# Optimization experiments

Hardware: AMD Instinct MI355X
Metric: run time of the kernel (lower is better)

The kernel has to match this reference:

```python
import jax, jax.numpy as jnp
import numpy as np

PSP_SIZES = (1, 3, 6, 8)  # KV length S = 1 + 9 + 36 + 64 = 110
BN_EPS = 1e-5


def conv1x1(x, W, b):
    # x: [B,C,H,W], W: [O,C], b: [O] -> [B,O,H,W]
    return jnp.einsum('bchw,oc->bohw', x, W) + b[None, :, None, None]


def psp(f):
    # f: [B,C,H,W] -> [B,C,S]; H,W divisible by all sizes so adaptive pool == block mean
    B, C, H, W = f.shape
    priors = []
    for s in PSP_SIZES:
        p = f.reshape(B, C, s, H // s, s, W // s).mean(axis=(3, 5))  # [B,C,s,s]
        priors.append(p.reshape(B, C, s * s))
    return jnp.concatenate(priors, axis=-1)  # [B,C,S]


def setup_inputs() -> dict:
    key = jax.random.key(0)
    ks = jax.random.split(key, 8)
    B, C, H, W = 8, 512, 72, 72
    Kc, Vc = 256, 256
    return {
        'x': jax.random.normal(ks[0], (B, C, H, W), jnp.float32),
        'Wk': jax.random.normal(ks[1], (Kc, C), jnp.float32) * (1.0 / np.sqrt(C)),
        'bk': jax.random.normal(ks[2], (Kc,), jnp.float32) * 0.01,
        'gamma': jnp.ones((Kc,), jnp.float32),
        'beta': jnp.zeros((Kc,), jnp.float32),
        'rmean': jnp.zeros((Kc,), jnp.float32),
        'rvar': jax.random.uniform(ks[3], (Kc,), jnp.float32, 0.5, 1.5),
        'Wv': jax.random.normal(ks[4], (Vc, C), jnp.float32) * (1.0 / np.sqrt(C)),
        'bv': jax.random.normal(ks[5], (Vc,), jnp.float32) * 0.01,
        'Ww': jax.random.normal(ks[6], (C, Vc), jnp.float32) * (1.0 / np.sqrt(Vc)),
        'bw': jnp.zeros((C,), jnp.float32),
    }


def reference(x, Wk, bk, gamma, beta, rmean, rvar, Wv, bv, Ww, bw):
    B, C, H, W = x.shape
    Kc = Wk.shape[0]
    Vc = Wv.shape[0]
    # f_value: conv1x1, then PSP -> value [B,S,Vc]
    value = psp(conv1x1(x, Wv, bv)).transpose(0, 2, 1)
    # f_key == f_query: conv1x1 + BN(inference) + ReLU
    k = conv1x1(x, Wk, bk)
    inv = gamma / jnp.sqrt(rvar + BN_EPS)
    k = jax.nn.relu(k * inv[None, :, None, None] + (beta - rmean * inv)[None, :, None, None])
    query = k.reshape(B, Kc, H * W).transpose(0, 2, 1)  # [B,HW,Kc]
    keyt = psp(k)  # [B,Kc,S]
    sim = jnp.einsum('bnk,bks->bns', query, keyt) * (Kc ** -0.5)
    sim = jax.nn.softmax(sim, axis=-1)
    context = jnp.einsum('bns,bsv->bnv', sim, value)  # [B,HW,Vc]
    context = context.transpose(0, 2, 1).reshape(B, Vc, H, W)
    return conv1x1(context, Ww, bw)
```

## Files before the change

kernel.cpp:

```cpp
#include <hip/hip_runtime.h>
#include <hip/hip_bf16.h>

#define HW    5184
#define WIDTH 72
#define CIN   512
#define KC    256
#define VC    256
#define NS    110
#define NSP   112
#define SPV   128
#define BATCH 8

typedef unsigned short u16;
typedef unsigned int   u32;
typedef __attribute__((ext_vector_type(8))) short bf16x8;
typedef __attribute__((ext_vector_type(4))) float f32x4;

typedef const __attribute__((address_space(1))) u32* gp_t;
typedef __attribute__((address_space(3))) u32* lp_t;

__device__ __forceinline__ u32 f2bf1(float f) {
    u32 u = __float_as_uint(f);
    return (u + 0x7FFFu + ((u >> 16) & 1u)) >> 16;
}
__device__ __forceinline__ u32 pack2(float a, float b) {
    return f2bf1(a) | (f2bf1(b) << 16);
}

__global__ void prep_kernel(const float* __restrict__ bk, const float* __restrict__ gamma,
                            const float* __restrict__ beta, const float* __restrict__ rmean,
                            const float* __restrict__ rvar, float* __restrict__ inv_out,
                            float* __restrict__ bc_out) {
    int i = threadIdx.x;
    float inv = gamma[i] * rsqrtf(rvar[i] + 1e-5f);
    inv_out[i] = inv;
    bc_out[i]  = bk[i] * inv + beta[i] - rmean[i] * inv;
}

__global__ __launch_bounds__(256) void cvt_w_kernel(
    const float* __restrict__ Wk, const float* __restrict__ Ww, const float* __restrict__ Wv,
    u16* __restrict__ Wkbf, u16* __restrict__ Wwbf, u16* __restrict__ Wvbf)
{
    int j = (blockIdx.x * 256 + threadIdx.x) * 4;
    const float* s; u16* d;
    if (j < KC * CIN)          { s = Wk; d = Wkbf; }
    else if (j < 2 * KC * CIN) { j -= KC * CIN;     s = Ww; d = Wwbf; }
    else                       { j -= 2 * KC * CIN; s = Wv; d = Wvbf; }
    float4 v = *(const float4*)&s[j];
    uint2 u;
    u.x = pack2(v.x, v.y);
    u.y = pack2(v.z, v.w);
    *(uint2*)&d[j] = u;
}

__global__ __launch_bounds__(256) void transpose_cvt_kernel(
    const float* __restrict__ in, u16* __restrict__ out, int C)
{
    const int z  = blockIdx.z;
    const int n0 = blockIdx.x * 32;
    const int k0 = blockIdx.y * 32;
    __shared__ float t[32][33];
    const int tx = threadIdx.x & 31, ty = threadIdx.x >> 5;
    const float* src = in + ((size_t)z * C + k0) * HW + n0;
#pragma unroll
    for (int i = 0; i < 4; i++)
        t[ty + i * 8][tx] = src[(size_t)(ty + i * 8) * HW + tx];
    __syncthreads();
    u16* dst = out + ((size_t)z * HW + n0) * C + k0;
    const int kp  = (threadIdx.x & 15) * 2;
    const int nl0 = threadIdx.x >> 4;
#pragma unroll
    for (int j = 0; j < 2; j++) {
        int nl = nl0 + j * 16;
        u32 u = pack2(t[kp][nl], t[kp + 1][nl]);
        *(u32*)&dst[(size_t)nl * C + kp] = u;
    }
}

__global__ __launch_bounds__(256) void gemm_nt_bf16(
    const u16* __restrict__ A, const u16* __restrict__ B, float* __restrict__ C,
    u16* __restrict__ Ct,
    int M, int N, int K, int nbx, int nby,
    const float* __restrict__ scale, const float* __restrict__ bias, int relu)
{
    const int tot = nbx * nby * BATCH;
    const int q = tot >> 3, r = tot & 7;
    const int xcd = blockIdx.x & 7;
    const int wg  = (xcd < r ? xcd * (q + 1) : r * (q + 1) + (xcd - r) * q) + (blockIdx.x >> 3);
    const int mb_ = wg % nby;
    const int nb_ = (wg / nby) % nbx;
    const int z   = wg / (nby * nbx);

    const int n0 = nb_ * 128;
    const int m0 = mb_ * 128;
    const size_t boff = (size_t)z * N * K;
    const size_t coff = (size_t)z * M * N;
    const int tid  = threadIdx.x;
    const int wid  = tid >> 6;
    const int lane = tid & 63;

    __shared__ __align__(16) u16 As[3][4][128][8];
    __shared__ __align__(16) u16 Bs[3][4][128][8];

    const int kg0  = (wid & 1) * 2;
    const int half = (wid >> 1) * 64;

    const u16* gA = A + (size_t)(m0 + half + lane) * K + kg0 * 8;
    int nIdx = n0 + half + lane;
    if (nIdx > N - 1) nIdx = N - 1;
    const u16* gB = B + boff + (size_t)nIdx * K + kg0 * 8;

    const int wm  = (wid >> 1) * 64;
    const int wn  = (wid & 1) * 64;
    const int l16 = lane & 15;
    const int lq  = lane >> 4;

    f32x4 acc[4][4];
#pragma unroll
    for (int mi = 0; mi < 4; mi++)
#pragma unroll
        for (int ni = 0; ni < 4; ni++)
            acc[mi][ni] = (f32x4){0.f, 0.f, 0.f, 0.f};

#define STAGE(d, kk)                                                                              \
    __builtin_amdgcn_global_load_lds((gp_t)(gA + (kk)),     (lp_t)&As[d][kg0][half][0], 16, 0, 0);\
    __builtin_amdgcn_global_load_lds((gp_t)(gA + (kk) + 8), (lp_t)&As[d][kg0+1][half][0],16, 0, 0);\
    __builtin_amdgcn_global_load_lds((gp_t)(gB + (kk)),     (lp_t)&Bs[d][kg0][half][0], 16, 0, 0);\
    __builtin_amdgcn_global_load_lds((gp_t)(gB + (kk) + 8), (lp_t)&Bs[d][kg0+1][half][0],16, 0, 0);

    const int NT = K >> 5;
    STAGE(0, 0)
    STAGE(1, 32)

    int cur = 0;
    for (int t = 0; t < NT; ++t) {
        if (t + 1 < NT) { asm volatile("s_waitcnt vmcnt(4)" ::: "memory"); }
        else            { asm volatile("s_waitcnt vmcnt(0)" ::: "memory"); }
        __builtin_amdgcn_s_barrier();
        __builtin_amdgcn_sched_barrier(0);

        if (t + 2 < NT) {
            int nb = cur + 2; if (nb >= 3) nb -= 3;
            STAGE(nb, (t + 2) * 32)
        }

        bf16x8 af[4], bf[4];
#pragma unroll
        for (int i = 0; i < 4; i++) {
            af[i] = *(const bf16x8*)&As[cur][lq][wm + i * 16 + l16][0];
            bf[i] = *(const bf16x8*)&Bs[cur][lq][wn + i * 16 + l16][0];
        }
        __builtin_amdgcn_s_setprio(1);
#pragma unroll
        for (int mi = 0; mi < 4; mi++)
#pragma unroll
            for (int ni = 0; ni < 4; ni++)
                acc[mi][ni] = __builtin_amdgcn_mfma_f32_16x16x32_bf16(
                    af[mi], bf[ni], acc[mi][ni], 0, 0, 0);
        __builtin_amdgcn_s_setprio(0);

        cur = (cur == 2) ? 0 : cur + 1;
    }
#undef STAGE

#pragma unroll
    for (int mi = 0; mi < 4; mi++) {
        const int mb = m0 + wm + mi * 16 + lq * 4;
        float sc[4], bi[4];
#pragma unroll
        for (int r2 = 0; r2 < 4; r2++) {
            sc[r2] = scale ? scale[mb + r2] : 1.0f;
            bi[r2] = bias  ? bias[mb + r2]  : 0.0f;
        }
#pragma unroll
        for (int ni = 0; ni < 4; ni++) {
            const int n = n0 + wn + ni * 16 + l16;
            if (n < N) {
                float v[4];
#pragma unroll
                for (int r2 = 0; r2 < 4; r2++) {
                    v[r2] = acc[mi][ni][r2] * sc[r2] + bi[r2];
                    if (relu) v[r2] = fmaxf(v[r2], 0.f);
                    C[coff + (size_t)(mb + r2) * N + n] = v[r2];
                }
                if (Ct) {
                    uint2 u;
                    u.x = pack2(v[0], v[1]);
                    u.y = pack2(v[2], v[3]);
                    *(uint2*)&Ct[(size_t)z * N * M + (size_t)n * M + mb] = u;
                }
            }
        }
    }
}

__global__ __launch_bounds__(256) void value_mfma_kernel(
    const u16* __restrict__ A, const u16* __restrict__ Bp,
    const float* __restrict__ bv, u16* __restrict__ valT)
{
    const int m0 = blockIdx.x * 128;
    const int b  = blockIdx.y;
    const int tid  = threadIdx.x;
    const int wid  = tid >> 6;
    const int lane = tid & 63;

    __shared__ __align__(16) u16 As[4][128][8];
    __shared__ __align__(16) u16 Bs[4][128][8];

    const int kg0  = (wid & 1) * 2;
    const int half = (wid >> 1) * 64;

    const u16* gA = A + (size_t)(m0 + half + lane) * CIN + kg0 * 8;
    const u16* gB = Bp + (size_t)b * SPV * CIN + (size_t)(half + lane) * CIN + kg0 * 8;

    lp_t lA0 = (lp_t)&As[kg0][half][0];
    lp_t lA1 = (lp_t)&As[kg0 + 1][half][0];
    lp_t lB0 = (lp_t)&Bs[kg0][half][0];
    lp_t lB1 = (lp_t)&Bs[kg0 + 1][half][0];

    const int wm  = (wid >> 1) * 64;
    const int wn  = (wid & 1) * 64;
    const int l16 = lane & 15;
    const int lq  = lane >> 4;

    f32x4 acc[4][4];
#pragma unroll
    for (int mi = 0; mi < 4; mi++)
#pragma unroll
        for (int ni = 0; ni < 4; ni++)
            acc[mi][ni] = (f32x4){0.f, 0.f, 0.f, 0.f};

    for (int k0 = 0; k0 < CIN; k0 += 32) {
        __builtin_amdgcn_global_load_lds((gp_t)(gA + k0),     lA0, 16, 0, 0);
        __builtin_amdgcn_global_load_lds((gp_t)(gA + k0 + 8), lA1, 16, 0, 0);
        __builtin_amdgcn_global_load_lds((gp_t)(gB + k0),     lB0, 16, 0, 0);
        __builtin_amdgcn_global_load_lds((gp_t)(gB + k0 + 8), lB1, 16, 0, 0);
        __syncthreads();

        bf16x8 af[4], bf[4];
#pragma unroll
        for (int i = 0; i < 4; i++) {
            af[i] = *(const bf16x8*)&As[lq][wm + i * 16 + l16][0];
            bf[i] = *(const bf16x8*)&Bs[lq][wn + i * 16 + l16][0];
        }
#pragma unroll
        for (int mi = 0; mi < 4; mi++)
#pragma unroll
            for (int ni = 0; ni < 4; ni++)
                acc[mi][ni] = __builtin_amdgcn_mfma_f32_16x16x32_bf16(
                    af[mi], bf[ni], acc[mi][ni], 0, 0, 0);
        __syncthreads();
    }

    char* vb = (char*)valT + (size_t)b * VC * SPV * 2;
#pragma unroll
    for (int mi = 0; mi < 4; mi++) {
        const int mb = m0 + wm + mi * 16 + lq * 4;
        float bi[4];
#pragma unroll
        for (int r = 0; r < 4; r++) bi[r] = bv[mb + r];
#pragma unroll
        for (int ni = 0; ni < 4; ni++) {
            const int n = wn + ni * 16 + l16;
#pragma unroll
            for (int r = 0; r < 4; r++) {
                const int v = mb + r;
                const int byte = v * 256 + ((n * 2) ^ ((v & 7) << 4));
                *(u16*)(vb + byte) = (u16)f2bf1(acc[mi][ni][r] + bi[r]);
            }
        }
    }
}

__global__ __launch_bounds__(128) void psp_pool_px_kernel(
    const float* __restrict__ in, u16* __restrict__ out)
{
    const int c = blockIdx.x;
    const int b = blockIdx.y;
    const int t = threadIdx.x;
    __shared__ float4 row4[1296];
    __shared__ float aux[100];
    float* row = (float*)row4;
    const float* src = in + ((size_t)b * CIN + c) * HW;
    for (int idx = t; idx < 1296; idx += 128)
        row4[idx] = *(const float4*)(src + idx * 4);
    __syncthreads();
    if (t < 64) {
        int r0 = (t >> 3) * 9, c0 = (t & 7) * 9;
        float s = 0.f;
        for (int i = 0; i < 9; i++)
            for (int j = 0; j < 9; j++) s += row[(r0 + i) * WIDTH + c0 + j];
        aux[t] = s;
    } else if (t < 100) {
        int tt = t - 64;
        int r0 = (tt / 6) * 12, c0 = (tt % 6) * 12;
        float s = 0.f;
        for (int i = 0; i < 12; i++)
            for (int j = 0; j < 12; j++) s += row[(r0 + i) * WIDTH + c0 + j];
        aux[64 + tt] = s;
    }
    __syncthreads();
    u16* ob = out + (size_t)b * SPV * CIN + c;
    if (t < 64) ob[(size_t)(46 + t) * CIN] = (u16)f2bf1(aux[t] * (1.f / 81.f));
    if (t < 36) ob[(size_t)(10 + t) * CIN] = (u16)f2bf1(aux[64 + t] * (1.f / 144.f));
    if (t < 9) {
        int r = t / 3, cc = t % 3;
        float s4 = aux[64 + (2 * r) * 6 + 2 * cc] + aux[64 + (2 * r) * 6 + 2 * cc + 1]
                 + aux[64 + (2 * r + 1) * 6 + 2 * cc] + aux[64 + (2 * r + 1) * 6 + 2 * cc + 1];
        ob[(size_t)(1 + t) * CIN] = (u16)f2bf1(s4 * (1.f / 576.f));
    }
    if (t == 0) {
        float s = 0.f;
        for (int i = 0; i < 64; i++) s += aux[i];
        ob[0] = (u16)f2bf1(s * (1.f / 5184.f));
    }
    if (t < 18) ob[(size_t)(110 + t) * CIN] = 0;
}

__global__ __launch_bounds__(128) void psp_pool_bf16_kernel(
    const float* __restrict__ in, u16* __restrict__ out)
{
    const int c = blockIdx.x;
    const int b = blockIdx.y;
    const int t = threadIdx.x;
    __shared__ float4 row4[1296];
    __shared__ float aux[100];
    float* row = (float*)row4;
    const float* src = in + ((size_t)b * KC + c) * HW;
    for (int idx = t; idx < 1296; idx += 128)
        row4[idx] = *(const float4*)(src + idx * 4);
    __syncthreads();
    if (t < 64) {
        int r0 = (t >> 3) * 9, c0 = (t & 7) * 9;
        float s = 0.f;
        for (int i = 0; i < 9; i++)
            for (int j = 0; j < 9; j++) s += row[(r0 + i) * WIDTH + c0 + j];
        aux[t] = s;
    } else if (t < 100) {
        int tt = t - 64;
        int r0 = (tt / 6) * 12, c0 = (tt % 6) * 12;
        float s = 0.f;
        for (int i = 0; i < 12; i++)
            for (int j = 0; j < 12; j++) s += row[(r0 + i) * WIDTH + c0 + j];
        aux[64 + tt] = s;
    }
    __syncthreads();
    char* ob = (char*)out + (size_t)b * NSP * KC * 2;
    const int c2 = c * 2;
#define KWR(S, V) *(u16*)(ob + (S) * 512 + (c2 ^ (((S) & 7) << 4))) = (u16)f2bf1(V)
    if (t < 64) KWR(46 + t, aux[t] * (1.f / 81.f));
    if (t < 36) KWR(10 + t, aux[64 + t] * (1.f / 144.f));
    if (t < 9) {
        int r = t / 3, cc = t % 3;
        float s4 = aux[64 + (2 * r) * 6 + 2 * cc] + aux[64 + (2 * r) * 6 + 2 * cc + 1]
                 + aux[64 + (2 * r + 1) * 6 + 2 * cc] + aux[64 + (2 * r + 1) * 6 + 2 * cc + 1];
        KWR(1 + t, s4 * (1.f / 576.f));
    }
    if (t == 0) {
        float s = 0.f;
        for (int i = 0; i < 64; i++) s += aux[i];
        KWR(0, s * (1.f / 5184.f));
        KWR(110, 0.f);
        KWR(111, 0.f);
    }
#undef KWR
}

__global__ __launch_bounds__(256) void attn_mfma_kernel(
    const u16* __restrict__ qT, const u16* __restrict__ keyt,
    const u16* __restrict__ valT, const u16* __restrict__ Wwb,
    const float* __restrict__ bw, float* __restrict__ out)
{
    const int b    = blockIdx.y;
    const int tid  = threadIdx.x;
    const int wid  = tid >> 6;
    const int lane = tid & 63;
    const int l16  = lane & 15;
    const int lq   = lane >> 4;
    const int nblk = blockIdx.x * 64;
    const int px0  = nblk + wid * 16;

    __shared__ __align__(16) u16 SM[61440];
    char* base = (char*)SM;
    const int VOFF = 57344;

    {
        const char* gk = (const char*)keyt + (size_t)b * (NSP * KC * 2);
        const char* gv = (const char*)valT + (size_t)b * (VC * SPV * 2);
#pragma unroll
        for (int i = 0; i < 14; i++) {
            const int o = (wid * 14 + i) * 1024;
            __builtin_amdgcn_global_load_lds((gp_t)(gk + o + lane * 16), (lp_t)(base + o), 16, 0, 0);
        }
#pragma unroll
        for (int i = 0; i < 16; i++) {
            const int o = (wid * 16 + i) * 1024;
            __builtin_amdgcn_global_load_lds((gp_t)(gv + o + lane * 16), (lp_t)(base + VOFF + o), 16, 0, 0);
        }
    }

    const u16* qrow = qT + ((size_t)b * HW + px0 + l16) * KC + lq * 8;
    bf16x8 aq[8];
#pragma unroll
    for (int ks = 0; ks < 8; ks++) aq[ks] = *(const bf16x8*)(qrow + ks * 32);

    __syncthreads();

    f32x4 acc[7];
#pragma unroll
    for (int ni = 0; ni < 7; ni++) acc[ni] = (f32x4){0.f, 0.f, 0.f, 0.f};
#pragma unroll
    for (int ks = 0; ks < 8; ks++) {
#pragma unroll
        for (int ni = 0; ni < 7; ni++) {
            const int s = ni * 16 + l16;
            const int byte = s * 512 + ((ks * 64 + lq * 16) ^ ((s & 7) << 4));
            bf16x8 bk = *(const bf16x8*)(base + byte);
            acc[ni] = __builtin_amdgcn_mfma_f32_16x16x32_bf16(aq[ks], bk, acc[ni], 0, 0, 0);
        }
    }
    if (l16 >= 14) acc[6] = (f32x4){-1e30f, -1e30f, -1e30f, -1e30f};

    float mx[4], sm[4], rn[4];
#pragma unroll
    for (int r = 0; r < 4; r++) {
        float m = acc[0][r];
#pragma unroll
        for (int ni = 1; ni < 7; ni++) m = fmaxf(m, acc[ni][r]);
        m = fmaxf(m, __shfl_xor(m, 1));
        m = fmaxf(m, __shfl_xor(m, 2));
        m = fmaxf(m, __shfl_xor(m, 4));
        m = fmaxf(m, __shfl_xor(m, 8));
        mx[r] = m * 0.0625f;
        sm[r] = 0.f;
    }

    __syncthreads();

    const int prow = wid * 16 + 4 * lq;
#pragma unroll
    for (int ni = 0; ni < 7; ni++) {
#pragma unroll
        for (int r = 0; r < 4; r++) {
            float p = __expf(acc[ni][r] * 0.0625f - mx[r]);
            sm[r] += p;
            const int row = prow + r;
            const int byte = row * 256 + (((ni * 16 + l16) * 2) ^ ((row & 7) << 4));
            *(u16*)(base + byte) = (u16)f2bf1(p);
        }
    }
    if (l16 < 2) {
#pragma unroll
        for (int r = 0; r < 4; r++) {
            const int row = prow + r;
            const int byte = row * 256 + ((224 + l16 * 16) ^ ((row & 7) << 4));
            *(bf16x8*)(base + byte) = (bf16x8){0, 0, 0, 0, 0, 0, 0, 0};
        }
    }
#pragma unroll
    for (int r = 0; r < 4; r++) {
        float s = sm[r];
        s += __shfl_xor(s, 1);
        s += __shfl_xor(s, 2);
        s += __shfl_xor(s, 4);
        s += __shfl_xor(s, 8);
        rn[r] = 1.f / s;
    }

    __syncthreads();

    f32x4 acc2[16];
#pragma unroll
    for (int ni = 0; ni < 16; ni++) acc2[ni] = (f32x4){0.f, 0.f, 0.f, 0.f};
    const int arow = wid * 16 + l16;
    const int aswz = (arow & 7) << 4;
#pragma unroll
    for (int ks = 0; ks < 4; ks++) {
        const int pbyte = arow * 256 + ((ks * 64 + lq * 16) ^ aswz);
        bf16x8 pa = *(const bf16x8*)(base + pbyte);
#pragma unroll
        for (int ni = 0; ni < 16; ni++) {
            const int v = ni * 16 + l16;
            const int vbyte = VOFF + v * 256 + ((ks * 64 + lq * 16) ^ ((v & 7) << 4));
            bf16x8 bvv = *(const bf16x8*)(base + vbyte);
            acc2[ni] = __builtin_amdgcn_mfma_f32_16x16x32_bf16(pa, bvv, acc2[ni], 0, 0, 0);
        }
    }

    __syncthreads();

#pragma unroll
    for (int ni = 0; ni < 16; ni++) {
#pragma unroll
        for (int r = 0; r < 4; r++) {
            const int row = prow + r;
            const int v = ni * 16 + l16;
            const int byte = row * 512 + ((v * 2) ^ ((row & 7) << 4));
            *(u16*)(base + byte) = (u16)f2bf1(acc2[ni][r] * rn[r]);
        }
    }
    __syncthreads();

    const int wc0 = wid * 128;
    f32x4 accg[4][8];
#pragma unroll
    for (int pi = 0; pi < 4; pi++)
#pragma unroll
        for (int cj = 0; cj < 8; cj++)
            accg[pi][cj] = (f32x4){0.f, 0.f, 0.f, 0.f};

    const u16* wwbase = Wwb + (size_t)(wc0 + l16) * VC + lq * 8;
#pragma unroll
    for (int ks = 0; ks < 8; ks++) {
        bf16x8 af[4];
#pragma unroll
        for (int pi = 0; pi < 4; pi++) {
            const int px = pi * 16 + l16;
            const int byte = px * 512 + ((ks * 64 + lq * 16) ^ ((px & 7) << 4));
            af[pi] = *(const bf16x8*)(base + byte);
        }
        bf16x8 bfr[8];
#pragma unroll
        for (int cj = 0; cj < 8; cj++)
            bfr[cj] = *(const bf16x8*)(wwbase + (size_t)cj * 16 * VC + ks * 32);
#pragma unroll
        for (int pi = 0; pi < 4; pi++)
#pragma unroll
            for (int cj = 0; cj < 8; cj++)
                accg[pi][cj] = __builtin_amdgcn_mfma_f32_16x16x32_bf16(
                    af[pi], bfr[cj], accg[pi][cj], 0, 0, 0);
    }

    char* scr = base + VOFF + wid * 16384;
    float* outb = out + (size_t)b * CIN * HW + nblk;
#pragma unroll
    for (int ci = 0; ci < 4; ci++) {
#pragma unroll
        for (int cjh = 0; cjh < 2; cjh++) {
            const int cj = ci * 2 + cjh;
            const int cl = cjh * 16 + l16;
            const int swz = (cl & 7) << 5;
#pragma unroll
            for (int pi = 0; pi < 4; pi++)
#pragma unroll
                for (int r = 0; r < 4; r++) {
                    const int px = pi * 16 + 4 * lq + r;
                    *(float*)(scr + cl * 256 + ((px * 4) ^ swz)) = accg[pi][cj][r];
                }
        }
#pragma unroll
        for (int cr = 0; cr < 8; cr++) {
            const int cl = cr * 4 + lq;
            const int swz = (cl & 7) << 5;
            float4 vv = *(const float4*)(scr + cl * 256 + ((l16 * 16) ^ swz));
            const int c = wc0 + ci * 32 + cl;
            const float bb = bw[c];
            vv.x += bb; vv.y += bb; vv.z += bb; vv.w += bb;
            *(float4*)&outb[(size_t)c * HW + l16 * 4] = vv;
        }
    }
}

extern "C" void kernel_launch(void* const* d_in, const int* in_sizes, int n_in,
                              void* d_out, int out_size, void* d_ws, size_t ws_size,
                              hipStream_t stream)
{
    const float* x     = (const float*)d_in[0];
    const float* Wk    = (const float*)d_in[1];
    const float* bk    = (const float*)d_in[2];
    const float* gamma = (const float*)d_in[3];
    const float* beta  = (const float*)d_in[4];
    const float* rmean = (const float*)d_in[5];
    const float* rvar  = (const float*)d_in[6];
    const float* Wv    = (const float*)d_in[7];
    const float* bv    = (const float*)d_in[8];
    const float* Ww    = (const float*)d_in[9];
    const float* bw    = (const float*)d_in[10];
    float* out = (float*)d_out;

    float* ws    = (float*)d_ws;
    float* k_ws  = ws;
    u16*   xT    = (u16*)(k_ws + (size_t)BATCH * KC * HW);
    u16*   kT    = xT + (size_t)BATCH * HW * CIN;
    u16*   pxb   = kT + (size_t)BATCH * HW * KC;
    u16*   keytb = pxb + (size_t)BATCH * SPV * CIN;
    u16*   valT  = keytb + (size_t)BATCH * NSP * KC;
    u16*   Wkbf  = valT + (size_t)BATCH * VC * SPV;
    u16*   Wwbf  = Wkbf + (size_t)KC * CIN;
    u16*   Wvbf  = Wwbf + (size_t)CIN * VC;
    float* inv   = (float*)(Wvbf + (size_t)KC * CIN);
    float* bc    = inv + 256;

    prep_kernel<<<1, 256, 0, stream>>>(bk, gamma, beta, rmean, rvar, inv, bc);
    cvt_w_kernel<<<384, 256, 0, stream>>>(Wk, Ww, Wv, Wkbf, Wwbf, Wvbf);
    psp_pool_px_kernel<<<dim3(CIN, BATCH), 128, 0, stream>>>(x, pxb);
    transpose_cvt_kernel<<<dim3(HW / 32, CIN / 32, BATCH), 256, 0, stream>>>(x, xT, CIN);
    {
        const int nbx = (HW + 127) / 128, nby = KC / 128;
        gemm_nt_bf16<<<nbx * nby * BATCH, 256, 0, stream>>>(
            Wkbf, xT, k_ws, kT, KC, HW, CIN, nbx, nby, inv, bc, 1);
    }
    psp_pool_bf16_kernel<<<dim3(KC, BATCH), 128, 0, stream>>>(k_ws, keytb);
    value_mfma_kernel<<<dim3(2, BATCH), 256, 0, stream>>>(Wvbf, pxb, bv, valT);
    attn_mfma_kernel<<<dim3(HW / 64, BATCH), 256, 0, stream>>>(
        kT, keytb, valT, Wwbf, bw, out);
}
```

Baseline: 178.1 us.

## Read value operand from global memory and shrink attention LDS for two blocks/CU

The value tile is no longer staged into LDS in the attention kernel. The P·V MFMA reads B fragments straight from global memory, so the projection kernel now writes valT in plain row-major layout instead of the swizzled one. Softmax probabilities get their own LDS region, the output scratch is shrunk, and two per-wave-local barriers are removed. Together these cut shared memory to about 72 KB so two blocks can share a CU. In exchange, value fragments come from L2/global with no swizzle, which may add load latency to the second GEMM.

```diff
diff --git a/kernel.cpp b/kernel.cpp
--- a/kernel.cpp
+++ b/kernel.cpp
@@ -252,7 +252,7 @@
         __syncthreads();
     }
 
-    char* vb = (char*)valT + (size_t)b * VC * SPV * 2;
+    u16* vb = valT + (size_t)b * VC * SPV;
 #pragma unroll
     for (int mi = 0; mi < 4; mi++) {
         const int mb = m0 + wm + mi * 16 + lq * 4;
@@ -263,11 +263,8 @@
         for (int ni = 0; ni < 4; ni++) {
             const int n = wn + ni * 16 + l16;
 #pragma unroll
-            for (int r = 0; r < 4; r++) {
-                const int v = mb + r;
-                const int byte = v * 256 + ((n * 2) ^ ((v & 7) << 4));
-                *(u16*)(vb + byte) = (u16)f2bf1(acc[mi][ni][r] + bi[r]);
-            }
+            for (int r = 0; r < 4; r++)
+                vb[(size_t)(mb + r) * SPV + n] = (u16)f2bf1(acc[mi][ni][r] + bi[r]);
         }
     }
 }
@@ -366,7 +363,7 @@
 #undef KWR
 }
 
-__global__ __launch_bounds__(256) void attn_mfma_kernel(
+__global__ __launch_bounds__(256, 2) void attn_mfma_kernel(
     const u16* __restrict__ qT, const u16* __restrict__ keyt,
     const u16* __restrict__ valT, const u16* __restrict__ Wwb,
     const float* __restrict__ bw, float* __restrict__ out)
@@ -380,22 +377,16 @@
     const int nblk = blockIdx.x * 64;
     const int px0  = nblk + wid * 16;
 
-    __shared__ __align__(16) u16 SM[61440];
+    __shared__ __align__(16) u16 SM[36864];
     char* base = (char*)SM;
-    const int VOFF = 57344;
+    const int POFF = 57344;
 
     {
         const char* gk = (const char*)keyt + (size_t)b * (NSP * KC * 2);
-        const char* gv = (const char*)valT + (size_t)b * (VC * SPV * 2);
 #pragma unroll
         for (int i = 0; i < 14; i++) {
             const int o = (wid * 14 + i) * 1024;
             __builtin_amdgcn_global_load_lds((gp_t)(gk + o + lane * 16), (lp_t)(base + o), 16, 0, 0);
-        }
-#pragma unroll
-        for (int i = 0; i < 16; i++) {
-            const int o = (wid * 16 + i) * 1024;
-            __builtin_amdgcn_global_load_lds((gp_t)(gv + o + lane * 16), (lp_t)(base + VOFF + o), 16, 0, 0);
         }
     }
 
@@ -435,8 +426,6 @@
         sm[r] = 0.f;
     }
 
-    __syncthreads();
-
     const int prow = wid * 16 + 4 * lq;
 #pragma unroll
     for (int ni = 0; ni < 7; ni++) {
@@ -445,7 +434,7 @@
             float p = __expf(acc[ni][r] * 0.0625f - mx[r]);
             sm[r] += p;
             const int row = prow + r;
-            const int byte = row * 256 + (((ni * 16 + l16) * 2) ^ ((row & 7) << 4));
+            const int byte = POFF + row * 256 + (((ni * 16 + l16) * 2) ^ ((row & 7) << 4));
             *(u16*)(base + byte) = (u16)f2bf1(p);
         }
     }
@@ -453,7 +442,7 @@
 #pragma unroll
         for (int r = 0; r < 4; r++) {
             const int row = prow + r;
-            const int byte = row * 256 + ((224 + l16 * 16) ^ ((row & 7) << 4));
+            const int byte = POFF + row * 256 + ((224 + l16 * 16) ^ ((row & 7) << 4));
             *(bf16x8*)(base + byte) = (bf16x8){0, 0, 0, 0, 0, 0, 0, 0};
         }
     }
@@ -467,22 +456,19 @@
         rn[r] = 1.f / s;
     }
 
-    __syncthreads();
-
     f32x4 acc2[16];
 #pragma unroll
     for (int ni = 0; ni < 16; ni++) acc2[ni] = (f32x4){0.f, 0.f, 0.f, 0.f};
     const int arow = wid * 16 + l16;
     const int aswz = (arow & 7) << 4;
+    const u16* vrow = valT + (size_t)b * VC * SPV + (size_t)l16 * SPV + lq * 8;
 #pragma unroll
     for (int ks = 0; ks < 4; ks++) {
-        const int pbyte = arow * 256 + ((ks * 64 + lq * 16) ^ aswz);
+        const int pbyte = POFF + arow * 256 + ((ks * 64 + lq * 16) ^ aswz);
         bf16x8 pa = *(const bf16x8*)(base + pbyte);
 #pragma unroll
         for (int ni = 0; ni < 16; ni++) {
-            const int v = ni * 16 + l16;
-            const int vbyte = VOFF + v * 256 + ((ks * 64 + lq * 16) ^ ((v & 7) << 4));
-            bf16x8 bvv = *(const bf16x8*)(base + vbyte);
+            bf16x8 bvv = *(const bf16x8*)(vrow + (size_t)ni * 16 * SPV + ks * 32);
             acc2[ni] = __builtin_amdgcn_mfma_f32_16x16x32_bf16(pa, bvv, acc2[ni], 0, 0, 0);
         }
     }
@@ -531,7 +517,7 @@
                     af[pi], bfr[cj], accg[pi][cj], 0, 0, 0);
     }
 
-    char* scr = base + VOFF + wid * 16384;
+    char* scr = base + 32768 + wid * 8192;
     float* outb = out + (size_t)b * CIN * HW + nblk;
 #pragma unroll
     for (int ci = 0; ci < 4; ci++) {
```

After: 190.9 us. 7.2% more time.

## Halve attention LDS footprint via staged K/V loads; widen transpose tiles

Applied to the files above, without the earlier changes.

The attention kernel's shared-memory buffer shrinks from about 120KB to 80KB so two workgroups can be resident per CU, and launch_bounds(256,2) is added to match. To fit, the key and value matrices are loaded into LDS in two halves, with a sync and reload between the halves of each MFMA phase. The probability tile moves to its own region, which removes two barriers. The transpose/convert kernel also moves from 32x32 to 64x64 tiles. The trade-off is more barriers, serialized global-to-LDS reloads inside each workgroup, and possible register pressure from the occupancy bound.

```diff
diff --git a/kernel.cpp b/kernel.cpp
--- a/kernel.cpp
+++ b/kernel.cpp
@@ -57,21 +57,21 @@
     const float* __restrict__ in, u16* __restrict__ out, int C)
 {
     const int z  = blockIdx.z;
-    const int n0 = blockIdx.x * 32;
-    const int k0 = blockIdx.y * 32;
-    __shared__ float t[32][33];
-    const int tx = threadIdx.x & 31, ty = threadIdx.x >> 5;
+    const int n0 = blockIdx.x * 64;
+    const int k0 = blockIdx.y * 64;
+    __shared__ float t[64][65];
+    const int tx = threadIdx.x & 63, ty = threadIdx.x >> 6;
     const float* src = in + ((size_t)z * C + k0) * HW + n0;
 #pragma unroll
-    for (int i = 0; i < 4; i++)
-        t[ty + i * 8][tx] = src[(size_t)(ty + i * 8) * HW + tx];
+    for (int i = 0; i < 16; i++)
+        t[ty + i * 4][tx] = src[(size_t)(ty + i * 4) * HW + tx];
     __syncthreads();
     u16* dst = out + ((size_t)z * HW + n0) * C + k0;
-    const int kp  = (threadIdx.x & 15) * 2;
-    const int nl0 = threadIdx.x >> 4;
-#pragma unroll
-    for (int j = 0; j < 2; j++) {
-        int nl = nl0 + j * 16;
+    const int kp  = (threadIdx.x & 31) * 2;
+    const int nl0 = threadIdx.x >> 5;
+#pragma unroll
+    for (int j = 0; j < 8; j++) {
+        int nl = nl0 + j * 8;
         u32 u = pack2(t[kp][nl], t[kp + 1][nl]);
         *(u32*)&dst[(size_t)nl * C + kp] = u;
     }
@@ -366,7 +366,7 @@
 #undef KWR
 }
 
-__global__ __launch_bounds__(256) void attn_mfma_kernel(
+__global__ __launch_bounds__(256, 2) void attn_mfma_kernel(
     const u16* __restrict__ qT, const u16* __restrict__ keyt,
     const u16* __restrict__ valT, const u16* __restrict__ Wwb,
     const float* __restrict__ bw, float* __restrict__ out)
@@ -380,23 +380,23 @@
     const int nblk = blockIdx.x * 64;
     const int px0  = nblk + wid * 16;
 
-    __shared__ __align__(16) u16 SM[61440];
+    __shared__ __align__(16) u16 SM[40960];
     char* base = (char*)SM;
-    const int VOFF = 57344;
-
-    {
-        const char* gk = (const char*)keyt + (size_t)b * (NSP * KC * 2);
-        const char* gv = (const char*)valT + (size_t)b * (VC * SPV * 2);
-#pragma unroll
-        for (int i = 0; i < 14; i++) {
-            const int o = (wid * 14 + i) * 1024;
-            __builtin_amdgcn_global_load_lds((gp_t)(gk + o + lane * 16), (lp_t)(base + o), 16, 0, 0);
-        }
-#pragma unroll
-        for (int i = 0; i < 16; i++) {
-            const int o = (wid * 16 + i) * 1024;
-            __builtin_amdgcn_global_load_lds((gp_t)(gv + o + lane * 16), (lp_t)(base + VOFF + o), 16, 0, 0);
-        }
+    const int VBUF = 32768;
+    const int POFF = 65536;
+
+    const char* gk = (const char*)keyt + (size_t)b * (NSP * KC * 2);
+    const char* gv = (const char*)valT + (size_t)b * (VC * SPV * 2);
+
+#pragma unroll
+    for (int i = 0; i < 8; i++) {
+        const int o = (wid * 8 + i) * 1024;
+        __builtin_amdgcn_global_load_lds((gp_t)(gk + o + lane * 16), (lp_t)(base + o), 16, 0, 0);
+    }
+#pragma unroll
+    for (int i = 0; i < 8; i++) {
+        const int o = (wid * 8 + i) * 1024;
+        __builtin_amdgcn_global_load_lds((gp_t)(gv + o + lane * 16), (lp_t)(base + VBUF + o), 16, 0, 0);
     }
 
     const u16* qrow = qT + ((size_t)b * HW + px0 + l16) * KC + lq * 8;
@@ -412,9 +412,29 @@
 #pragma unroll
     for (int ks = 0; ks < 8; ks++) {
 #pragma unroll
-        for (int ni = 0; ni < 7; ni++) {
+        for (int ni = 0; ni < 4; ni++) {
             const int s = ni * 16 + l16;
             const int byte = s * 512 + ((ks * 64 + lq * 16) ^ ((s & 7) << 4));
+            bf16x8 bk = *(const bf16x8*)(base + byte);
+            acc[ni] = __builtin_amdgcn_mfma_f32_16x16x32_bf16(aq[ks], bk, acc[ni], 0, 0, 0);
+        }
+    }
+    __syncthreads();
+
+#pragma unroll
+    for (int i = 0; i < 6; i++) {
+        const int o = (wid * 6 + i) * 1024;
+        __builtin_amdgcn_global_load_lds((gp_t)(gk + 32768 + o + lane * 16), (lp_t)(base + o), 16, 0, 0);
+    }
+    __syncthreads();
+
+#pragma unroll
+    for (int ks = 0; ks < 8; ks++) {
+#pragma unroll
+        for (int ni = 4; ni < 7; ni++) {
+            const int s = ni * 16 + l16;
+            const int srow = s - 64;
+            const int byte = srow * 512 + ((ks * 64 + lq * 16) ^ ((srow & 7) << 4));
             bf16x8 bk = *(const bf16x8*)(base + byte);
             acc[ni] = __builtin_amdgcn_mfma_f32_16x16x32_bf16(aq[ks], bk, acc[ni], 0, 0, 0);
         }
@@ -435,8 +455,6 @@
         sm[r] = 0.f;
     }
 
-    __syncthreads();
-
     const int prow = wid * 16 + 4 * lq;
 #pragma unroll
     for (int ni = 0; ni < 7; ni++) {
@@ -445,7 +463,7 @@
             float p = __expf(acc[ni][r] * 0.0625f - mx[r]);
             sm[r] += p;
             const int row = prow + r;
-            const int byte = row * 256 + (((ni * 16 + l16) * 2) ^ ((row & 7) << 4));
+            const int byte = POFF + row * 256 + (((ni * 16 + l16) * 2) ^ ((row & 7) << 4));
             *(u16*)(base + byte) = (u16)f2bf1(p);
         }
     }
@@ -453,7 +471,7 @@
 #pragma unroll
         for (int r = 0; r < 4; r++) {
             const int row = prow + r;
-            const int byte = row * 256 + ((224 + l16 * 16) ^ ((row & 7) << 4));
+            const int byte = POFF + row * 256 + ((224 + l16 * 16) ^ ((row & 7) << 4));
             *(bf16x8*)(base + byte) = (bf16x8){0, 0, 0, 0, 0, 0, 0, 0};
         }
     }
@@ -467,8 +485,6 @@
         rn[r] = 1.f / s;
     }
 
-    __syncthreads();
-
     f32x4 acc2[16];
 #pragma unroll
     for (int ni = 0; ni < 16; ni++) acc2[ni] = (f32x4){0.f, 0.f, 0.f, 0.f};
@@ -476,17 +492,37 @@
     const int aswz = (arow & 7) << 4;
 #pragma unroll
     for (int ks = 0; ks < 4; ks++) {
-        const int pbyte = arow * 256 + ((ks * 64 + lq * 16) ^ aswz);
+        const int pbyte = POFF + arow * 256 + ((ks * 64 + lq * 16) ^ aswz);
         bf16x8 pa = *(const bf16x8*)(base + pbyte);
 #pragma unroll
-        for (int ni = 0; ni < 16; ni++) {
+        for (int ni = 0; ni < 8; ni++) {
             const int v = ni * 16 + l16;
-            const int vbyte = VOFF + v * 256 + ((ks * 64 + lq * 16) ^ ((v & 7) << 4));
+            const int vbyte = VBUF + v * 256 + ((ks * 64 + lq * 16) ^ ((v & 7) << 4));
             bf16x8 bvv = *(const bf16x8*)(base + vbyte);
             acc2[ni] = __builtin_amdgcn_mfma_f32_16x16x32_bf16(pa, bvv, acc2[ni], 0, 0, 0);
         }
     }
-
+    __syncthreads();
+
+#pragma unroll
+    for (int i = 0; i < 8; i++) {
+        const int o = (wid * 8 + i) * 1024;
+        __builtin_amdgcn_global_load_lds((gp_t)(gv + 32768 + o + lane * 16), (lp_t)(base + VBUF + o), 16, 0, 0);
+    }
+    __syncthreads();
+
+#pragma unroll
+    for (int ks = 0; ks < 4; ks++) {
+        const int pbyte = POFF + arow * 256 + ((ks * 64 + lq * 16) ^ aswz);
+        bf16x8 pa = *(const bf16x8*)(base + pbyte);
+#pragma unroll
+        for (int ni = 8; ni < 16; ni++) {
+            const int vrow = (ni - 8) * 16 + l16;
+            const int vbyte = VBUF + vrow * 256 + ((ks * 64 + lq * 16) ^ ((vrow & 7) << 4));
+            bf16x8 bvv = *(const bf16x8*)(base + vbyte);
+            acc2[ni] = __builtin_amdgcn_mfma_f32_16x16x32_bf16(pa, bvv, acc2[ni], 0, 0, 0);
+        }
+    }
     __syncthreads();
 
 #pragma unroll
@@ -531,7 +567,7 @@
                     af[pi], bfr[cj], accg[pi][cj], 0, 0, 0);
     }
 
-    char* scr = base + VOFF + wid * 16384;
+    char* scr = base + VBUF + wid * 8192;
     float* outb = out + (size_t)b * CIN * HW + nblk;
 #pragma unroll
     for (int ci = 0; ci < 4; ci++) {
@@ -594,7 +630,7 @@
     prep_kernel<<<1, 256, 0, stream>>>(bk, gamma, beta, rmean, rvar, inv, bc);
     cvt_w_kernel<<<384, 256, 0, stream>>>(Wk, Ww, Wv, Wkbf, Wwbf, Wvbf);
     psp_pool_px_kernel<<<dim3(CIN, BATCH), 128, 0, stream>>>(x, pxb);
-    transpose_cvt_kernel<<<dim3(HW / 32, CIN / 32, BATCH), 256, 0, stream>>>(x, xT, CIN);
+    transpose_cvt_kernel<<<dim3(HW / 64, CIN / 64, BATCH), 256, 0, stream>>>(x, xT, CIN);
     {
         const int nbx = (HW + 127) / 128, nby = KC / 128;
         gemm_nt_bf16<<<nbx * nby * BATCH, 256, 0, stream>>>(
```

After: 177.0 us. No clear change (-0.6%).
